# Kernel optimization log

Hardware: AMD Instinct MI355X
Metric: run time of the kernel (lower is better)

## Reference

```python
import jax, jax.numpy as jnp
import numpy as np

MASK_FILL = jnp.float32(-2**32 + 1)

def dice(x, alpha):
    # x: (S, B, F); batch-dim (dim=0) mean/std, unbiased std like torch.std
    avg = x.mean(axis=0)
    std = jnp.std(x, axis=0, ddof=1)
    p = jax.nn.sigmoid((x - avg) / std)
    return x * p + alpha * x * (1.0 - p)

def setup_inputs() -> dict:
    key = jax.random.key(0)
    ks = jax.random.split(key, 12)
    S, B, D = 200, 1024, 128          # seq_len, batch, 2H
    F = 4 * D                          # num_features = 512
    L1, L2 = 80, 40
    inp = {
        "query": jax.random.normal(ks[0], (B, D), jnp.float32),
        "facts": jax.random.normal(ks[1], (S, B, D), jnp.float32),
        "mask": jax.random.randint(ks[2], (S, B), 0, 2).astype(bool),
        "W1": jax.random.normal(ks[3], (F, L1), jnp.float32) / np.sqrt(F),
        "b1": jnp.zeros((L1,), jnp.float32),
        "a1": jnp.zeros((1,), jnp.float32),
        "W2": jax.random.normal(ks[4], (L1, L2), jnp.float32) / np.sqrt(L1),
        "b2": jnp.zeros((L2,), jnp.float32),
        "a2": jnp.zeros((1,), jnp.float32),
        "W3": jax.random.normal(ks[5], (L2, 1), jnp.float32) / np.sqrt(L2),
        "b3": jnp.zeros((1,), jnp.float32),
    }
    return inp

def reference(query, facts, mask, W1, b1, a1, W2, b2, a2, W3, b3):
    S, B, D = facts.shape
    # faithful to torch: tile along feature dim then reshape (permutes elements)
    q2 = jnp.tile(query, (1, S)).reshape(S, B, D)
    x = jnp.concatenate([q2, facts, q2 * facts, q2 - facts], axis=-1)  # (S,B,4D)
    h = dice(jnp.einsum('sbf,fl->sbl', x, W1) + b1, a1)
    h = dice(jnp.einsum('sbf,fl->sbl', h, W2) + b2, a2)
    logits = (jnp.einsum('sbf,fl->sbl', h, W3) + b3).squeeze(-1)  # (S,B)
    masked = jnp.where(mask, logits, MASK_FILL)
    normalized = jax.nn.softmax(masked, axis=0)
    return normalized[..., None] * facts  # (S,B,D)
```

## Files before the change

### kernel.cpp

```cpp
#include <hip/hip_runtime.h>
#include <hip/hip_bf16.h>
#include <math.h>

#define SS 200
#define BB 1024
#define DD 128
#define FF 512
#define LL1 80
#define LL2 40
#define PP (SS*BB)
#define MASK_FILL_F (-4294967295.0f)
#define NTILE 13

typedef short bf16x8 __attribute__((ext_vector_type(8)));
typedef float f32x4  __attribute__((ext_vector_type(4)));

static __device__ __forceinline__ unsigned short f2bf(float x) {
    __hip_bfloat16 h = __float2bfloat16(x);
    return *reinterpret_cast<unsigned short*>(&h);
}
static __device__ __forceinline__ float bf2f(unsigned short u) {
    __hip_bfloat16 h = *reinterpret_cast<__hip_bfloat16*>(&u);
    return __bfloat162float(h);
}
static __device__ __forceinline__ void split8(const float* x, bf16x8& ah, bf16x8& al) {
#pragma unroll
    for (int j = 0; j < 8; ++j) {
        unsigned u = __float_as_uint(x[j]);
        ah[j] = (short)(u >> 16);
        float hi = __uint_as_float(u & 0xffff0000u);
        al[j] = (short)f2bf(x[j] - hi);
    }
}

__global__ void k_prep_all(const float* __restrict__ W1, const float* __restrict__ W2,
                           const unsigned char* __restrict__ mask,
                           unsigned short* __restrict__ bfr1,
                           unsigned short* __restrict__ bfr2, int* __restrict__ flag) {
    const int blk = blockIdx.x;
    if (blk == 35) {
        if (threadIdx.x == 0) {
            int f = 0;
            for (int i = 0; i < 256; ++i)
                if ((i & 3) && mask[i]) f = 1;
            *flag = f;
        }
        return;
    }
    if (blk < 30) {
        int t = blk * 256 + threadIdx.x;
        if (t >= 120 * 64) return;
        int lane = t & 63;
        int fid  = t >> 6;
        int nt   = fid % 5;
        int hl   = (fid / 5) % 2;
        int step = (fid / 10) % 6;
        int h    = fid / 60;
        int ktL  = step / 3;
        int seg  = step - 3 * ktL;
        int kt   = h * 2 + ktL;
        int n     = nt * 16 + (lane & 15);
        int kbase = kt * 32 + (lane >> 4) * 8;
        unsigned short* o = bfr1 + (size_t)t * 8;
#pragma unroll
        for (int j = 0; j < 8; ++j) {
            int k = kbase + j;
            float w;
            if (seg == 0)      w = W1[k * LL1 + n] + W1[(384 + k) * LL1 + n];
            else if (seg == 1) w = W1[(128 + k) * LL1 + n] - W1[(384 + k) * LL1 + n];
            else               w = W1[(256 + k) * LL1 + n];
            unsigned short hb = f2bf(w);
            o[j] = (hl == 0) ? hb : f2bf(w - bf2f(hb));
        }
    } else {
        int t = (blk - 30) * 256 + threadIdx.x;
        if (t >= 18 * 64) return;
        int lane = t & 63;
        int fid  = t >> 6;
        int hl   = fid & 1;
        int nt   = (fid >> 1) % 3;
        int kt   = fid / 6;
        int n  = nt * 16 + (lane & 15);
        int kb = kt * 32 + (lane >> 4) * 8;
        unsigned short* o = bfr2 + (size_t)t * 8;
#pragma unroll
        for (int j = 0; j < 8; ++j) {
            int k = kb + j;
            float w = (k < LL1 && n < LL2) ? W2[k * LL2 + n] : 0.f;
            unsigned short hb = f2bf(w);
            o[j] = (hl == 0) ? hb : f2bf(w - bf2f(hb));
        }
    }
}

__global__ __launch_bounds__(256, 2) void k_fused(
    const float* __restrict__ query, const float* __restrict__ facts,
    const unsigned short* __restrict__ bfr1, const unsigned short* __restrict__ bfr2,
    const float* __restrict__ b1, const float* __restrict__ a1,
    const float* __restrict__ b2, const float* __restrict__ a2,
    const float* __restrict__ W3, const float* __restrict__ b3,
    const void* __restrict__ mask, const int* __restrict__ flag,
    float* __restrict__ out) {
    const int tid  = threadIdx.x;
    const int w    = tid >> 6;
    const int lane = tid & 63;
    const int m    = lane & 15;
    const int quad = lane >> 4;
    const int b    = blockIdx.x;

    __shared__ __align__(16) float z1f[NTILE * 16 * 81 + 16];
    __shared__ float psum[240], pssq[240];
    __shared__ float smean[LL1], sistd[LL1];
    __shared__ float sw3[LL2];
    __shared__ float red[4];
    __shared__ float wgt[SS];

    int tile[4], pr[4], qr[4];
    bool tl[4];
#pragma unroll
    for (int t = 0; t < 4; ++t) {
        tile[t] = t * 4 + w;
        tl[t]   = (tile[t] < NTILE);
        int s = tile[t] * 16 + m;
        if (s > SS - 1) s = SS - 1;
        pr[t] = s * BB + b;
        qr[t] = pr[t] / SS;
    }

    f32x4 acc[4][5];
#pragma unroll
    for (int t = 0; t < 4; ++t)
#pragma unroll
        for (int nt = 0; nt < 5; ++nt) acc[t][nt] = (f32x4){0.f, 0.f, 0.f, 0.f};

#pragma unroll 1
    for (int h = 0; h < 2; ++h) {
        if (h) __syncthreads();
        {
            const int4* src = (const int4*)bfr1 + h * 3840 + tid;
            int4* dst = (int4*)z1f;
#pragma unroll
            for (int it = 0; it < 15; ++it)
                dst[it * 256 + tid] = src[it * 256];
        }
        __syncthreads();
        const unsigned short* lbuf = (const unsigned short*)z1f;
#pragma unroll
        for (int ktL = 0; ktL < 2; ++ktL) {
            const int dbase = (h * 2 + ktL) * 32 + quad * 8;
#pragma unroll
            for (int tp = 0; tp < 2; ++tp) {
                float q8[2][8], f8[2][8];
#pragma unroll
                for (int u = 0; u < 2; ++u) {
                    const int t = tp * 2 + u;
                    const float* qp = query + (size_t)qr[t] * DD + dbase;
                    const float* fp = facts + (size_t)pr[t] * DD + dbase;
                    *(float4*)&q8[u][0] = *(const float4*)qp;
                    *(float4*)&q8[u][4] = *(const float4*)(qp + 4);
                    *(float4*)&f8[u][0] = *(const float4*)fp;
                    *(float4*)&f8[u][4] = *(const float4*)(fp + 4);
                }
#pragma unroll
                for (int seg = 0; seg < 3; ++seg) {
                    const int step = ktL * 3 + seg;
                    bf16x8 Bh[5], Bl[5];
#pragma unroll
                    for (int nt = 0; nt < 5; ++nt) {
                        Bh[nt] = *(const bf16x8*)&lbuf[((step * 2 + 0) * 5 + nt) * 512 + lane * 8];
                        Bl[nt] = *(const bf16x8*)&lbuf[((step * 2 + 1) * 5 + nt) * 512 + lane * 8];
                    }
#pragma unroll
                    for (int u = 0; u < 2; ++u) {
                        const int t = tp * 2 + u;
                        if (!tl[t]) continue;
                        float x8[8];
#pragma unroll
                        for (int j = 0; j < 8; ++j)
                            x8[j] = (seg == 0) ? q8[u][j]
                                  : (seg == 1 ? f8[u][j] : q8[u][j] * f8[u][j]);
                        bf16x8 ah, al;
                        split8(x8, ah, al);
#pragma unroll
                        for (int nt = 0; nt < 5; ++nt) {
                            acc[t][nt] = __builtin_amdgcn_mfma_f32_16x16x32_bf16(ah, Bh[nt], acc[t][nt], 0, 0, 0);
                            acc[t][nt] = __builtin_amdgcn_mfma_f32_16x16x32_bf16(al, Bh[nt], acc[t][nt], 0, 0, 0);
                            acc[t][nt] = __builtin_amdgcn_mfma_f32_16x16x32_bf16(ah, Bl[nt], acc[t][nt], 0, 0, 0);
                        }
                    }
                }
            }
        }
    }

    __syncthreads();
    {
        float b1v[5];
#pragma unroll
        for (int nt = 0; nt < 5; ++nt) b1v[nt] = b1[nt * 16 + m];
#pragma unroll
        for (int t = 0; t < 4; ++t) {
            if (!tl[t]) continue;
#pragma unroll
            for (int nt = 0; nt < 5; ++nt)
#pragma unroll
                for (int r = 0; r < 4; ++r)
                    z1f[(tile[t] * 16 + quad * 4 + r) * 81 + nt * 16 + m] = acc[t][nt][r] + b1v[nt];
        }
    }
    __syncthreads();

    if (tid < 240) {
        const int l = tid % LL1, c = tid / LL1;
        const int s0 = c * 67, s1 = (c == 2) ? SS : s0 + 67;
        float sum = 0.f, ssq = 0.f;
        for (int s = s0; s < s1; ++s) {
            float v = z1f[s * 81 + l];
            sum += v;
            ssq = fmaf(v, v, ssq);
        }
        psum[c * LL1 + l] = sum;
        pssq[c * LL1 + l] = ssq;
    }
    __syncthreads();
    if (tid < LL1) {
        float sum = psum[tid] + psum[LL1 + tid] + psum[2 * LL1 + tid];
        float ssq = pssq[tid] + pssq[LL1 + tid] + pssq[2 * LL1 + tid];
        float mn  = sum * (1.f / SS);
        float var = (ssq - (float)SS * mn * mn) * (1.f / (SS - 1));
        smean[tid] = mn;
        sistd[tid] = rsqrtf(var);
    }
    __syncthreads();

    const float alpha1 = *a1;
    f32x4 acc2[4][3];
#pragma unroll
    for (int t = 0; t < 4; ++t)
#pragma unroll
        for (int nt = 0; nt < 3; ++nt) acc2[t][nt] = (f32x4){0.f, 0.f, 0.f, 0.f};

#pragma unroll
    for (int kt = 0; kt < 3; ++kt) {
        bf16x8 Bh[3], Bl[3];
#pragma unroll
        for (int nt = 0; nt < 3; ++nt) {
            Bh[nt] = *(const bf16x8*)(bfr2 + (size_t)((kt * 3 + nt) * 2 + 0) * 512 + lane * 8);
            Bl[nt] = *(const bf16x8*)(bfr2 + (size_t)((kt * 3 + nt) * 2 + 1) * 512 + lane * 8);
        }
        const int kb = kt * 32 + quad * 8;
        const bool lv = (kt < 2 || quad < 2);
#pragma unroll
        for (int t = 0; t < 4; ++t) {
            if (!tl[t]) continue;
            float x8[8];
            if (lv) {
                const float* zr = &z1f[(tile[t] * 16 + m) * 81 + kb];
#pragma unroll
                for (int j = 0; j < 8; ++j) {
                    float v  = zr[j];
                    float pp = 1.f / (1.f + expf(-(v - smean[kb + j]) * sistd[kb + j]));
                    x8[j] = v * (alpha1 + (1.f - alpha1) * pp);
                }
            } else {
#pragma unroll
                for (int j = 0; j < 8; ++j) x8[j] = 0.f;
            }
            bf16x8 ah, al;
            split8(x8, ah, al);
#pragma unroll
            for (int nt = 0; nt < 3; ++nt) {
                acc2[t][nt] = __builtin_amdgcn_mfma_f32_16x16x32_bf16(ah, Bh[nt], acc2[t][nt], 0, 0, 0);
                acc2[t][nt] = __builtin_amdgcn_mfma_f32_16x16x32_bf16(al, Bh[nt], acc2[t][nt], 0, 0, 0);
                acc2[t][nt] = __builtin_amdgcn_mfma_f32_16x16x32_bf16(ah, Bl[nt], acc2[t][nt], 0, 0, 0);
            }
        }
    }
    __syncthreads();

    {
        float b2v[3];
#pragma unroll
        for (int nt = 0; nt < 3; ++nt) {
            const int n = nt * 16 + m;
            b2v[nt] = (n < LL2) ? b2[n] : 0.f;
        }
#pragma unroll
        for (int t = 0; t < 4; ++t) {
            if (!tl[t]) continue;
#pragma unroll
            for (int r = 0; r < 4; ++r) {
                const int srow = tile[t] * 16 + quad * 4 + r;
                if (srow >= SS) continue;
#pragma unroll
                for (int nt = 0; nt < 3; ++nt) {
                    const int n = nt * 16 + m;
                    if (n < LL2) z1f[srow * 41 + n] = acc2[t][nt][r] + b2v[nt];
                }
            }
        }
    }
    __syncthreads();

    if (tid < 240) {
        const int l = tid % LL2, c = tid / LL2;
        const int s0 = c * 34, s1 = (c == 5) ? SS : s0 + 34;
        float sum = 0.f, ssq = 0.f;
        for (int s = s0; s < s1; ++s) {
            float v = z1f[s * 41 + l];
            sum += v;
            ssq = fmaf(v, v, ssq);
        }
        psum[c * LL2 + l] = sum;
        pssq[c * LL2 + l] = ssq;
    }
    __syncthreads();
    if (tid < LL2) {
        float sum = 0.f, ssq = 0.f;
#pragma unroll
        for (int c = 0; c < 6; ++c) {
            sum += psum[c * LL2 + tid];
            ssq += pssq[c * LL2 + tid];
        }
        float mn  = sum * (1.f / SS);
        float var = (ssq - (float)SS * mn * mn) * (1.f / (SS - 1));
        smean[tid] = mn;
        sistd[tid] = rsqrtf(var);
        sw3[tid]   = W3[tid];
    }
    __syncthreads();

    const float alpha2 = *a2;
    const int boolLayout = *flag;
    float logit = -3.0e38f;
    if (tid < SS) {
        float dot = b3[0];
#pragma unroll
        for (int k = 0; k < LL2; ++k) {
            float v  = z1f[tid * 41 + k];
            float pp = 1.f / (1.f + expf(-(v - smean[k]) * sistd[k]));
            float hh = v * (pp + alpha2 * (1.f - pp));
            dot = fmaf(hh, sw3[k], dot);
        }
        const int mi = tid * BB + b;
        const bool mk = boolLayout ? (((const unsigned char*)mask)[mi] != 0)
                                   : (((const int*)mask)[mi] != 0);
        logit = mk ? dot : MASK_FILL_F;
    }
    float v = logit;
#pragma unroll
    for (int off = 1; off < 64; off <<= 1) v = fmaxf(v, __shfl_xor(v, off, 64));
    if ((tid & 63) == 0) red[tid >> 6] = v;
    __syncthreads();
    const float smax = fmaxf(fmaxf(red[0], red[1]), fmaxf(red[2], red[3]));
    __syncthreads();
    const float e = (tid < SS) ? expf(logit - smax) : 0.f;
    v = e;
#pragma unroll
    for (int off = 1; off < 64; off <<= 1) v += __shfl_xor(v, off, 64);
    if ((tid & 63) == 0) red[tid >> 6] = v;
    __syncthreads();
    const float inv = 1.f / (red[0] + red[1] + red[2] + red[3]);
    if (tid < SS) wgt[tid] = e * inv;
    __syncthreads();

    const float4* f4 = (const float4*)facts;
    float4* o4 = (float4*)out;
#pragma unroll 5
    for (int i = tid; i < SS * 32; i += 256) {
        const int s  = i >> 5;
        const int d4 = i & 31;
        const size_t idx = (size_t)(s * BB + b) * 32 + d4;
        float4 f = f4[idx];
        const float ww = wgt[s];
        float4 o;
        o.x = f.x * ww; o.y = f.y * ww; o.z = f.z * ww; o.w = f.w * ww;
        o4[idx] = o;
    }
}

extern "C" void kernel_launch(void* const* d_in, const int* in_sizes, int n_in,
                              void* d_out, int out_size, void* d_ws, size_t ws_size,
                              hipStream_t stream) {
    const float* query = (const float*)d_in[0];
    const float* facts = (const float*)d_in[1];
    const void*  mask  = d_in[2];
    const float* W1 = (const float*)d_in[3];
    const float* b1 = (const float*)d_in[4];
    const float* a1 = (const float*)d_in[5];
    const float* W2 = (const float*)d_in[6];
    const float* b2 = (const float*)d_in[7];
    const float* a2 = (const float*)d_in[8];
    const float* W3 = (const float*)d_in[9];
    const float* b3 = (const float*)d_in[10];

    unsigned short* bfr1 = (unsigned short*)d_ws;
    unsigned short* bfr2 = (unsigned short*)((char*)d_ws + 131072);
    int* flag = (int*)((char*)d_ws + 163840);

    k_prep_all<<<36, 256, 0, stream>>>(W1, W2, (const unsigned char*)mask, bfr1, bfr2, flag);
    k_fused<<<BB, 256, 0, stream>>>(query, facts, bfr1, bfr2, b1, a1, b2, a2,
                                    W3, b3, mask, flag, (float*)d_out);
}
```

Measured before the change: 319.7 us.

## Use 512-thread blocks, split facts scaling into separate kernel, fast sigmoid

Blocks grow from 256 to 512 threads, so each wave now owns 2 tiles instead of 4 and the dice reductions split across more partial sums. The final softmax-weighted scaling of facts moves from the fused kernel into a separate fully parallel elementwise kernel. The fused kernel now only writes a per-batch weight buffer, which the new kernel reads. Sigmoid and exp use the fast `__expf` and `rcp` intrinsics, and the mask-layout flag check becomes a wave ballot. The weight matrices are staged in the tail of the output buffer, relying on stream ordering; this adds an extra kernel launch and a second full read of facts, and loses some precision in the softmax and sigmoid.

```diff
diff --git a/kernel.cpp b/kernel.cpp
--- a/kernel.cpp
+++ b/kernel.cpp
@@ -32,6 +32,9 @@
         al[j] = (short)f2bf(x[j] - hi);
     }
 }
+static __device__ __forceinline__ float fast_sigmoid(float t) {
+    return __builtin_amdgcn_rcpf(1.f + __expf(-t));
+}
 
 __global__ void k_prep_all(const float* __restrict__ W1, const float* __restrict__ W2,
                            const unsigned char* __restrict__ mask,
@@ -39,11 +42,11 @@
                            unsigned short* __restrict__ bfr2, int* __restrict__ flag) {
     const int blk = blockIdx.x;
     if (blk == 35) {
-        if (threadIdx.x == 0) {
-            int f = 0;
-            for (int i = 0; i < 256; ++i)
-                if ((i & 3) && mask[i]) f = 1;
-            *flag = f;
+        if (threadIdx.x < 64) {
+            const uchar4 u = ((const uchar4*)mask)[threadIdx.x];
+            const bool f = ((u.y | u.z) | u.w) != 0;
+            const unsigned long long anyf = __ballot(f);
+            if (threadIdx.x == 0) *flag = (anyf != 0ull) ? 1 : 0;
         }
         return;
     }
@@ -93,14 +96,14 @@
     }
 }
 
-__global__ __launch_bounds__(256, 2) void k_fused(
+__global__ __launch_bounds__(512, 4) void k_fused(
     const float* __restrict__ query, const float* __restrict__ facts,
     const unsigned short* __restrict__ bfr1, const unsigned short* __restrict__ bfr2,
     const float* __restrict__ b1, const float* __restrict__ a1,
     const float* __restrict__ b2, const float* __restrict__ a2,
     const float* __restrict__ W3, const float* __restrict__ b3,
     const void* __restrict__ mask, const int* __restrict__ flag,
-    float* __restrict__ out) {
+    float* __restrict__ wbufT) {
     const int tid  = threadIdx.x;
     const int w    = tid >> 6;
     const int lane = tid & 63;
@@ -109,17 +112,16 @@
     const int b    = blockIdx.x;
 
     __shared__ __align__(16) float z1f[NTILE * 16 * 81 + 16];
-    __shared__ float psum[240], pssq[240];
+    __shared__ float psum[480], pssq[480];
     __shared__ float smean[LL1], sistd[LL1];
     __shared__ float sw3[LL2];
-    __shared__ float red[4];
-    __shared__ float wgt[SS];
-
-    int tile[4], pr[4], qr[4];
-    bool tl[4];
-#pragma unroll
-    for (int t = 0; t < 4; ++t) {
-        tile[t] = t * 4 + w;
+    __shared__ float red[8];
+
+    int tile[2], pr[2], qr[2];
+    bool tl[2];
+#pragma unroll
+    for (int t = 0; t < 2; ++t) {
+        tile[t] = t * 8 + w;
         tl[t]   = (tile[t] < NTILE);
         int s = tile[t] * 16 + m;
         if (s > SS - 1) s = SS - 1;
@@ -127,9 +129,9 @@
         qr[t] = pr[t] / SS;
     }
 
-    f32x4 acc[4][5];
-#pragma unroll
-    for (int t = 0; t < 4; ++t)
+    f32x4 acc[2][5];
+#pragma unroll
+    for (int t = 0; t < 2; ++t)
 #pragma unroll
         for (int nt = 0; nt < 5; ++nt) acc[t][nt] = (f32x4){0.f, 0.f, 0.f, 0.f};
 
@@ -137,56 +139,54 @@
     for (int h = 0; h < 2; ++h) {
         if (h) __syncthreads();
         {
-            const int4* src = (const int4*)bfr1 + h * 3840 + tid;
+            const int4* src = (const int4*)bfr1 + h * 3840;
             int4* dst = (int4*)z1f;
 #pragma unroll
-            for (int it = 0; it < 15; ++it)
-                dst[it * 256 + tid] = src[it * 256];
+            for (int it = 0; it < 8; ++it) {
+                int idx = it * 512 + tid;
+                if (idx < 3840) dst[idx] = src[idx];
+            }
         }
         __syncthreads();
         const unsigned short* lbuf = (const unsigned short*)z1f;
 #pragma unroll
         for (int ktL = 0; ktL < 2; ++ktL) {
             const int dbase = (h * 2 + ktL) * 32 + quad * 8;
-#pragma unroll
-            for (int tp = 0; tp < 2; ++tp) {
-                float q8[2][8], f8[2][8];
-#pragma unroll
-                for (int u = 0; u < 2; ++u) {
-                    const int t = tp * 2 + u;
-                    const float* qp = query + (size_t)qr[t] * DD + dbase;
-                    const float* fp = facts + (size_t)pr[t] * DD + dbase;
-                    *(float4*)&q8[u][0] = *(const float4*)qp;
-                    *(float4*)&q8[u][4] = *(const float4*)(qp + 4);
-                    *(float4*)&f8[u][0] = *(const float4*)fp;
-                    *(float4*)&f8[u][4] = *(const float4*)(fp + 4);
+            float q8[2][8], f8[2][8];
+#pragma unroll
+            for (int t = 0; t < 2; ++t) {
+                if (!tl[t]) continue;
+                const float* qp = query + (size_t)qr[t] * DD + dbase;
+                const float* fp = facts + (size_t)pr[t] * DD + dbase;
+                *(float4*)&q8[t][0] = *(const float4*)qp;
+                *(float4*)&q8[t][4] = *(const float4*)(qp + 4);
+                *(float4*)&f8[t][0] = *(const float4*)fp;
+                *(float4*)&f8[t][4] = *(const float4*)(fp + 4);
+            }
+#pragma unroll
+            for (int seg = 0; seg < 3; ++seg) {
+                const int step = ktL * 3 + seg;
+                bf16x8 Bh[5], Bl[5];
+#pragma unroll
+                for (int nt = 0; nt < 5; ++nt) {
+                    Bh[nt] = *(const bf16x8*)&lbuf[((step * 2 + 0) * 5 + nt) * 512 + lane * 8];
+                    Bl[nt] = *(const bf16x8*)&lbuf[((step * 2 + 1) * 5 + nt) * 512 + lane * 8];
                 }
 #pragma unroll
-                for (int seg = 0; seg < 3; ++seg) {
-                    const int step = ktL * 3 + seg;
-                    bf16x8 Bh[5], Bl[5];
+                for (int t = 0; t < 2; ++t) {
+                    if (!tl[t]) continue;
+                    float x8[8];
+#pragma unroll
+                    for (int j = 0; j < 8; ++j)
+                        x8[j] = (seg == 0) ? q8[t][j]
+                              : (seg == 1 ? f8[t][j] : q8[t][j] * f8[t][j]);
+                    bf16x8 ah, al;
+                    split8(x8, ah, al);
 #pragma unroll
                     for (int nt = 0; nt < 5; ++nt) {
-                        Bh[nt] = *(const bf16x8*)&lbuf[((step * 2 + 0) * 5 + nt) * 512 + lane * 8];
-                        Bl[nt] = *(const bf16x8*)&lbuf[((step * 2 + 1) * 5 + nt) * 512 + lane * 8];
-                    }
-#pragma unroll
-                    for (int u = 0; u < 2; ++u) {
-                        const int t = tp * 2 + u;
-                        if (!tl[t]) continue;
-                        float x8[8];
-#pragma unroll
-                        for (int j = 0; j < 8; ++j)
-                            x8[j] = (seg == 0) ? q8[u][j]
-                                  : (seg == 1 ? f8[u][j] : q8[u][j] * f8[u][j]);
-                        bf16x8 ah, al;
-                        split8(x8, ah, al);
-#pragma unroll
-                        for (int nt = 0; nt < 5; ++nt) {
-                            acc[t][nt] = __builtin_amdgcn_mfma_f32_16x16x32_bf16(ah, Bh[nt], acc[t][nt], 0, 0, 0);
-                            acc[t][nt] = __builtin_amdgcn_mfma_f32_16x16x32_bf16(al, Bh[nt], acc[t][nt], 0, 0, 0);
-                            acc[t][nt] = __builtin_amdgcn_mfma_f32_16x16x32_bf16(ah, Bl[nt], acc[t][nt], 0, 0, 0);
-                        }
+                        acc[t][nt] = __builtin_amdgcn_mfma_f32_16x16x32_bf16(ah, Bh[nt], acc[t][nt], 0, 0, 0);
+                        acc[t][nt] = __builtin_amdgcn_mfma_f32_16x16x32_bf16(al, Bh[nt], acc[t][nt], 0, 0, 0);
+                        acc[t][nt] = __builtin_amdgcn_mfma_f32_16x16x32_bf16(ah, Bl[nt], acc[t][nt], 0, 0, 0);
                     }
                 }
             }
@@ -199,7 +199,7 @@
 #pragma unroll
         for (int nt = 0; nt < 5; ++nt) b1v[nt] = b1[nt * 16 + m];
 #pragma unroll
-        for (int t = 0; t < 4; ++t) {
+        for (int t = 0; t < 2; ++t) {
             if (!tl[t]) continue;
 #pragma unroll
             for (int nt = 0; nt < 5; ++nt)
@@ -210,9 +210,10 @@
     }
     __syncthreads();
 
-    if (tid < 240) {
+    if (tid < 480) {
         const int l = tid % LL1, c = tid / LL1;
-        const int s0 = c * 67, s1 = (c == 2) ? SS : s0 + 67;
+        const int s0 = c * 34;
+        const int s1 = (s0 + 34 < SS) ? s0 + 34 : SS;
         float sum = 0.f, ssq = 0.f;
         for (int s = s0; s < s1; ++s) {
             float v = z1f[s * 81 + l];
@@ -224,8 +225,12 @@
     }
     __syncthreads();
     if (tid < LL1) {
-        float sum = psum[tid] + psum[LL1 + tid] + psum[2 * LL1 + tid];
-        float ssq = pssq[tid] + pssq[LL1 + tid] + pssq[2 * LL1 + tid];
+        float sum = 0.f, ssq = 0.f;
+#pragma unroll
+        for (int c = 0; c < 6; ++c) {
+            sum += psum[c * LL1 + tid];
+            ssq += pssq[c * LL1 + tid];
+        }
         float mn  = sum * (1.f / SS);
         float var = (ssq - (float)SS * mn * mn) * (1.f / (SS - 1));
         smean[tid] = mn;
@@ -234,9 +239,9 @@
     __syncthreads();
 
     const float alpha1 = *a1;
-    f32x4 acc2[4][3];
-#pragma unroll
-    for (int t = 0; t < 4; ++t)
+    f32x4 acc2[2][3];
+#pragma unroll
+    for (int t = 0; t < 2; ++t)
 #pragma unroll
         for (int nt = 0; nt < 3; ++nt) acc2[t][nt] = (f32x4){0.f, 0.f, 0.f, 0.f};
 
@@ -251,7 +256,7 @@
         const int kb = kt * 32 + quad * 8;
         const bool lv = (kt < 2 || quad < 2);
 #pragma unroll
-        for (int t = 0; t < 4; ++t) {
+        for (int t = 0; t < 2; ++t) {
             if (!tl[t]) continue;
             float x8[8];
             if (lv) {
@@ -259,7 +264,7 @@
 #pragma unroll
                 for (int j = 0; j < 8; ++j) {
                     float v  = zr[j];
-                    float pp = 1.f / (1.f + expf(-(v - smean[kb + j]) * sistd[kb + j]));
+                    float pp = fast_sigmoid((v - smean[kb + j]) * sistd[kb + j]);
                     x8[j] = v * (alpha1 + (1.f - alpha1) * pp);
                 }
             } else {
@@ -286,7 +291,7 @@
             b2v[nt] = (n < LL2) ? b2[n] : 0.f;
         }
 #pragma unroll
-        for (int t = 0; t < 4; ++t) {
+        for (int t = 0; t < 2; ++t) {
             if (!tl[t]) continue;
 #pragma unroll
             for (int r = 0; r < 4; ++r) {
@@ -302,9 +307,10 @@
     }
     __syncthreads();
 
-    if (tid < 240) {
+    if (tid < 480) {
         const int l = tid % LL2, c = tid / LL2;
-        const int s0 = c * 34, s1 = (c == 5) ? SS : s0 + 34;
+        const int s0 = c * 17;
+        const int s1 = (s0 + 17 < SS) ? s0 + 17 : SS;
         float sum = 0.f, ssq = 0.f;
         for (int s = s0; s < s1; ++s) {
             float v = z1f[s * 41 + l];
@@ -318,7 +324,7 @@
     if (tid < LL2) {
         float sum = 0.f, ssq = 0.f;
 #pragma unroll
-        for (int c = 0; c < 6; ++c) {
+        for (int c = 0; c < 12; ++c) {
             sum += psum[c * LL2 + tid];
             ssq += pssq[c * LL2 + tid];
         }
@@ -338,7 +344,7 @@
 #pragma unroll
         for (int k = 0; k < LL2; ++k) {
             float v  = z1f[tid * 41 + k];
-            float pp = 1.f / (1.f + expf(-(v - smean[k]) * sistd[k]));
+            float pp = fast_sigmoid((v - smean[k]) * sistd[k]);
             float hh = v * (pp + alpha2 * (1.f - pp));
             dot = fmaf(hh, sw3[k], dot);
         }
@@ -352,31 +358,33 @@
     for (int off = 1; off < 64; off <<= 1) v = fmaxf(v, __shfl_xor(v, off, 64));
     if ((tid & 63) == 0) red[tid >> 6] = v;
     __syncthreads();
-    const float smax = fmaxf(fmaxf(red[0], red[1]), fmaxf(red[2], red[3]));
-    __syncthreads();
-    const float e = (tid < SS) ? expf(logit - smax) : 0.f;
+    float smax = red[0];
+#pragma unroll
+    for (int i = 1; i < 8; ++i) smax = fmaxf(smax, red[i]);
+    __syncthreads();
+    const float e = (tid < SS) ? __expf(logit - smax) : 0.f;
     v = e;
 #pragma unroll
     for (int off = 1; off < 64; off <<= 1) v += __shfl_xor(v, off, 64);
     if ((tid & 63) == 0) red[tid >> 6] = v;
     __syncthreads();
-    const float inv = 1.f / (red[0] + red[1] + red[2] + red[3]);
-    if (tid < SS) wgt[tid] = e * inv;
-    __syncthreads();
-
-    const float4* f4 = (const float4*)facts;
-    float4* o4 = (float4*)out;
-#pragma unroll 5
-    for (int i = tid; i < SS * 32; i += 256) {
-        const int s  = i >> 5;
-        const int d4 = i & 31;
-        const size_t idx = (size_t)(s * BB + b) * 32 + d4;
-        float4 f = f4[idx];
-        const float ww = wgt[s];
-        float4 o;
-        o.x = f.x * ww; o.y = f.y * ww; o.z = f.z * ww; o.w = f.w * ww;
-        o4[idx] = o;
-    }
+    float ssum = red[0];
+#pragma unroll
+    for (int i = 1; i < 8; ++i) ssum += red[i];
+    const float inv = __builtin_amdgcn_rcpf(ssum);
+    if (tid < SS) wbufT[(size_t)b * SS + tid] = e * inv;
+}
+
+__global__ __launch_bounds__(256) void k4_scale(
+    const float* __restrict__ wbufT, const float* __restrict__ facts,
+    float* __restrict__ out) {
+    int i = blockIdx.x * 256 + threadIdx.x;
+    int p = i >> 5;
+    float w = wbufT[(size_t)(p & (BB - 1)) * SS + (p >> 10)];
+    float4 f = ((const float4*)facts)[i];
+    float4 o;
+    o.x = f.x * w; o.y = f.y * w; o.z = f.z * w; o.w = f.w * w;
+    ((float4*)out)[i] = o;
 }
 
 extern "C" void kernel_launch(void* const* d_in, const int* in_sizes, int n_in,
@@ -393,12 +401,15 @@
     const float* a2 = (const float*)d_in[8];
     const float* W3 = (const float*)d_in[9];
     const float* b3 = (const float*)d_in[10];
-
-    unsigned short* bfr1 = (unsigned short*)d_ws;
-    unsigned short* bfr2 = (unsigned short*)((char*)d_ws + 131072);
-    int* flag = (int*)((char*)d_ws + 163840);
+    float* out = (float*)d_out;
+
+    unsigned short* bfr1 = (unsigned short*)(out + 24739840);
+    unsigned short* bfr2 = (unsigned short*)(out + 24801280);
+    float* wbufT = (float*)d_ws;
+    int*   flag  = (int*)((char*)d_ws + 900 * 1024);
 
     k_prep_all<<<36, 256, 0, stream>>>(W1, W2, (const unsigned char*)mask, bfr1, bfr2, flag);
-    k_fused<<<BB, 256, 0, stream>>>(query, facts, bfr1, bfr2, b1, a1, b2, a2,
-                                    W3, b3, mask, flag, (float*)d_out);
-}
+    k_fused<<<BB, 512, 0, stream>>>(query, facts, bfr1, bfr2, b1, a1, b2, a2,
+                                    W3, b3, mask, flag, wbufT);
+    k4_scale<<<(PP * DD) / (256 * 4), 256, 0, stream>>>(wbufT, facts, out);
+}
```

After: 328.9 us. 2.9% more time.
